# Performance work log

Hardware: AMD Instinct MI355X
Metric: run time of the kernel (lower is better)

Reference implementation:

```python
import jax, jax.numpy as jnp
import numpy as np

REG = 1e-4  # regularizer from __init__


def setup_inputs() -> dict:
    key = jax.random.key(0)
    k1, k2 = jax.random.split(key)
    data = jax.random.normal(k1, (131072, 64), dtype=jnp.float32)
    centers = jax.random.normal(k2, (512, 64), dtype=jnp.float32)
    return {"data": data, "centers": centers}


def reference(data, centers):
    # Pairwise squared Euclidean distances via GEMM: [N, K]
    d2 = (
        jnp.sum(data * data, axis=1, keepdims=True)
        + jnp.sum(centers * centers, axis=1)[None, :]
        - 2.0 * (data @ centers.T)
    )
    d2 = jnp.maximum(d2, 0.0)  # clamp numerical negatives
    r = jnp.sqrt(d2)
    # xlogy(r^2, r + reg) = r^2 * log(r + reg), defined as 0 where r^2 == 0
    rbfs = jnp.where(d2 > 0.0, d2 * jnp.log(r + REG), 0.0)
    ones = jnp.ones((data.shape[0], 1), dtype=data.dtype)
    return jnp.concatenate([ones, data, rbfs], axis=-1)  # [N, 1 + D + K]
```

## Files before the change

### kernel.cpp

```cpp
#include <hip/hip_runtime.h>

#define NROWS 131072
#define DDIM  64
#define KCTR  512
#define OUT_W 577
#define RPB   16
#define NTILES (NROWS / RPB)
#define SPAN_F32 (RPB * OUT_W)
#define SPAN_V4  (SPAN_F32 / 4)
#define GRID 768
#define K_HALF_LN2 0.34657359027997264f

typedef __attribute__((ext_vector_type(8))) short bfrag8;
typedef __attribute__((ext_vector_type(4))) float f32x4;

__device__ __forceinline__ short f2bf(float f) {
    union { float f; unsigned u; } v; v.f = f;
    return (short)((v.u + 0x8000u) >> 16);
}

__global__ __launch_bounds__(256, 3) void dicrbf_mfma(
    const float* __restrict__ data,
    const float* __restrict__ centers,
    float* __restrict__ out)
{
    __shared__ __align__(16) float s_span[SPAN_F32];
    __shared__ short s_dbf[RPB][72];
    __shared__ float s_xsq[RPB];
    __shared__ float s_cnorm[KCTR];

    const int t    = threadIdx.x;
    const int lane = t & 63;
    const int wid  = t >> 6;
    const int l15  = lane & 15;
    const int lhi  = lane >> 4;
    const int cbase = wid * 128;

    for (int k = t; k < KCTR; k += 256) {
        const f32x4* c4 = reinterpret_cast<const f32x4*>(centers + (size_t)k * DDIM);
        float s = 0.f;
#pragma unroll
        for (int i = 0; i < DDIM / 4; ++i) {
            f32x4 u = c4[i];
            s += u[0]*u[0] + u[1]*u[1] + u[2]*u[2] + u[3]*u[3];
        }
        s_cnorm[k] = s;
    }

    bfrag8 afr[8][2];
#pragma unroll
    for (int mf = 0; mf < 8; ++mf) {
        const float* cp = centers + (size_t)(cbase + mf * 16 + l15) * DDIM + lhi * 8;
#pragma unroll
        for (int ks = 0; ks < 2; ++ks) {
            const f32x4 u0 = *reinterpret_cast<const f32x4*>(cp + ks * 32);
            const f32x4 u1 = *reinterpret_cast<const f32x4*>(cp + ks * 32 + 4);
            bfrag8 fr;
            fr[0] = f2bf(u0[0]); fr[1] = f2bf(u0[1]); fr[2] = f2bf(u0[2]); fr[3] = f2bf(u0[3]);
            fr[4] = f2bf(u1[0]); fr[5] = f2bf(u1[1]); fr[6] = f2bf(u1[2]); fr[7] = f2bf(u1[3]);
            afr[mf][ks] = fr;
        }
    }
    __syncthreads();

    f32x4 cnr[8];
#pragma unroll
    for (int mf = 0; mf < 8; ++mf)
        cnr[mf] = *reinterpret_cast<const f32x4*>(&s_cnorm[cbase + mf * 16 + lhi * 4]);

    const int r  = t >> 4;
    const int jj = t & 15;

    size_t tile = blockIdx.x;
    f32x4 v;
    if (tile < NTILES)
        v = *reinterpret_cast<const f32x4*>(data + (tile * RPB + r) * DDIM + jj * 4);

    for (; tile < NTILES; tile += GRID) {
        __syncthreads();

        float s = v[0]*v[0] + v[1]*v[1] + v[2]*v[2] + v[3]*v[3];
        s += __shfl_xor(s, 1);
        s += __shfl_xor(s, 2);
        s += __shfl_xor(s, 4);
        s += __shfl_xor(s, 8);
        if (jj == 0) { s_xsq[r] = s; s_span[r * OUT_W] = 1.0f; }

        float* spv = &s_span[r * OUT_W + 1 + jj * 4];
        spv[0] = v[0]; spv[1] = v[1]; spv[2] = v[2]; spv[3] = v[3];

        short b4[4] = { f2bf(v[0]), f2bf(v[1]), f2bf(v[2]), f2bf(v[3]) };
        *reinterpret_cast<uint2*>(&s_dbf[r][jj * 4]) =
            *reinterpret_cast<const uint2*>(b4);

        {
            const size_t nt = tile + GRID;
            if (nt < NTILES)
                v = *reinterpret_cast<const f32x4*>(data + (nt * RPB + r) * DDIM + jj * 4);
        }
        __syncthreads();

        const bfrag8 b0 = *reinterpret_cast<const bfrag8*>(&s_dbf[l15][lhi * 8]);
        const bfrag8 b1 = *reinterpret_cast<const bfrag8*>(&s_dbf[l15][32 + lhi * 8]);
        const float xsq = s_xsq[l15];

#pragma unroll
        for (int mf = 0; mf < 8; ++mf) {
            f32x4 acc = (f32x4)(0.f);
            acc = __builtin_amdgcn_mfma_f32_16x16x32_bf16(afr[mf][0], b0, acc, 0, 0, 0);
            acc = __builtin_amdgcn_mfma_f32_16x16x32_bf16(afr[mf][1], b1, acc, 0, 0, 0);

            float* sp = &s_span[l15 * OUT_W + 1 + DDIM + cbase + mf * 16 + lhi * 4];
#pragma unroll
            for (int k = 0; k < 4; ++k) {
                float d2 = xsq + cnr[mf][k] - 2.0f * acc[k];
                d2 = fmaxf(d2, 0.0f);
                float w = (K_HALF_LN2 * d2) * __log2f(d2);
                sp[k] = (d2 > 0.0f) ? w : 0.0f;
            }
        }
        __syncthreads();

        const f32x4* sp4 = reinterpret_cast<const f32x4*>(s_span);
        f32x4* o4 = reinterpret_cast<f32x4*>(out) + tile * (size_t)SPAN_V4;
#pragma unroll 1
        for (int i = t; i < SPAN_V4; i += 256)
            o4[i] = sp4[i];
    }
}

extern "C" void kernel_launch(void* const* d_in, const int* in_sizes, int n_in,
                              void* d_out, int out_size, void* d_ws, size_t ws_size,
                              hipStream_t stream) {
    const float* data    = (const float*)d_in[0];
    const float* centers = (const float*)d_in[1];
    float* out = (float*)d_out;

    hipLaunchKernelGGL(dicrbf_mfma, dim3(GRID), dim3(256), 0, stream,
                       data, centers, out);
}
```

Measured before the change: 93.37 us.

## Double-buffer LDS output span and use lightweight LDS-only barriers

The LDS output span is now double-buffered, so one full block barrier per tile is dropped. The remaining barriers become a custom barrier that waits only on LDS counters, not on outstanding global stores. This lets the global stores of one tile overlap with the next tile's MFMA and log work. The grid drops to 512 blocks with an exact round count, occupancy is set to 2 blocks per CU to fit the doubled LDS, and the copy-out loop is fully unrolled. The cost is fewer resident waves per CU and more LDS per block.

```diff
diff --git a/kernel.cpp b/kernel.cpp
--- a/kernel.cpp
+++ b/kernel.cpp
@@ -8,7 +8,8 @@
 #define NTILES (NROWS / RPB)
 #define SPAN_F32 (RPB * OUT_W)
 #define SPAN_V4  (SPAN_F32 / 4)
-#define GRID 768
+#define GRID 512
+#define ROUNDS (NTILES / GRID)
 #define K_HALF_LN2 0.34657359027997264f
 
 typedef __attribute__((ext_vector_type(8))) short bfrag8;
@@ -19,12 +20,18 @@
     return (short)((v.u + 0x8000u) >> 16);
 }
 
-__global__ __launch_bounds__(256, 3) void dicrbf_mfma(
+__device__ __forceinline__ void lds_barrier() {
+    asm volatile("s_waitcnt lgkmcnt(0)" ::: "memory");
+    __builtin_amdgcn_s_barrier();
+    __builtin_amdgcn_sched_barrier(0);
+}
+
+__global__ __launch_bounds__(256, 2) void dicrbf_mfma(
     const float* __restrict__ data,
     const float* __restrict__ centers,
     float* __restrict__ out)
 {
-    __shared__ __align__(16) float s_span[SPAN_F32];
+    __shared__ __align__(16) float s_span[2][SPAN_F32];
     __shared__ short s_dbf[RPB][72];
     __shared__ float s_xsq[RPB];
     __shared__ float s_cnorm[KCTR];
@@ -72,33 +79,31 @@
     const int jj = t & 15;
 
     size_t tile = blockIdx.x;
-    f32x4 v;
-    if (tile < NTILES)
-        v = *reinterpret_cast<const f32x4*>(data + (tile * RPB + r) * DDIM + jj * 4);
+    f32x4 v = *reinterpret_cast<const f32x4*>(data + (tile * RPB + r) * DDIM + jj * 4);
 
-    for (; tile < NTILES; tile += GRID) {
-        __syncthreads();
+    int p = 0;
+    for (int round = 0; round < ROUNDS; ++round, tile += GRID, p ^= 1) {
+        float* span = s_span[p];
 
         float s = v[0]*v[0] + v[1]*v[1] + v[2]*v[2] + v[3]*v[3];
         s += __shfl_xor(s, 1);
         s += __shfl_xor(s, 2);
         s += __shfl_xor(s, 4);
         s += __shfl_xor(s, 8);
-        if (jj == 0) { s_xsq[r] = s; s_span[r * OUT_W] = 1.0f; }
+        if (jj == 0) { s_xsq[r] = s; span[r * OUT_W] = 1.0f; }
 
-        float* spv = &s_span[r * OUT_W + 1 + jj * 4];
+        float* spv = &span[r * OUT_W + 1 + jj * 4];
         spv[0] = v[0]; spv[1] = v[1]; spv[2] = v[2]; spv[3] = v[3];
 
         short b4[4] = { f2bf(v[0]), f2bf(v[1]), f2bf(v[2]), f2bf(v[3]) };
         *reinterpret_cast<uint2*>(&s_dbf[r][jj * 4]) =
             *reinterpret_cast<const uint2*>(b4);
 
-        {
-            const size_t nt = tile + GRID;
-            if (nt < NTILES)
-                v = *reinterpret_cast<const f32x4*>(data + (nt * RPB + r) * DDIM + jj * 4);
-        }
-        __syncthreads();
+        if (round + 1 < ROUNDS)
+            v = *reinterpret_cast<const f32x4*>(
+                data + ((tile + GRID) * RPB + r) * DDIM + jj * 4);
+
+        lds_barrier();
 
         const bfrag8 b0 = *reinterpret_cast<const bfrag8*>(&s_dbf[l15][lhi * 8]);
         const bfrag8 b1 = *reinterpret_cast<const bfrag8*>(&s_dbf[l15][32 + lhi * 8]);
@@ -110,7 +115,7 @@
             acc = __builtin_amdgcn_mfma_f32_16x16x32_bf16(afr[mf][0], b0, acc, 0, 0, 0);
             acc = __builtin_amdgcn_mfma_f32_16x16x32_bf16(afr[mf][1], b1, acc, 0, 0, 0);
 
-            float* sp = &s_span[l15 * OUT_W + 1 + DDIM + cbase + mf * 16 + lhi * 4];
+            float* sp = &span[l15 * OUT_W + 1 + DDIM + cbase + mf * 16 + lhi * 4];
 #pragma unroll
             for (int k = 0; k < 4; ++k) {
                 float d2 = xsq + cnr[mf][k] - 2.0f * acc[k];
@@ -119,13 +124,18 @@
                 sp[k] = (d2 > 0.0f) ? w : 0.0f;
             }
         }
-        __syncthreads();
 
-        const f32x4* sp4 = reinterpret_cast<const f32x4*>(s_span);
+        lds_barrier();
+
+        const f32x4* sp4 = reinterpret_cast<const f32x4*>(span);
         f32x4* o4 = reinterpret_cast<f32x4*>(out) + tile * (size_t)SPAN_V4;
-#pragma unroll 1
-        for (int i = t; i < SPAN_V4; i += 256)
-            o4[i] = sp4[i];
+#pragma unroll
+        for (int i = 0; i < 9; ++i) {
+            const int idx = t + i * 256;
+            o4[idx] = sp4[idx];
+        }
+        if (t < SPAN_V4 - 9 * 256)
+            o4[t + 9 * 256] = sp4[t + 9 * 256];
     }
 }
 
```

Result: faster. 85.34 us (-8.6%).
